# Performance work log

Hardware: AMD Instinct MI355X
Metric: run time of the kernel (lower is better)

The kernel has to match this reference:

```python
import jax, jax.numpy as jnp
import numpy as np
from jax import lax

EPS = 1e-05
Q = 4          # window size (hard-coded in BotBlock)
HEADS = 4
DIM = 16       # bottleneck(64) // heads(4)


def conv3x3(x, w, b):
    # x: [N,C,H,W], w: [O,I,3,3]
    y = lax.conv_general_dilated(x, w, (1, 1), ((1, 1), (1, 1)),
                                 dimension_numbers=('NCHW', 'OIHW', 'NCHW'))
    return y + b[None, :, None, None]


def batchnorm(x, gamma, beta):
    # training-mode BN: batch statistics over (N,H,W), biased variance
    m = jnp.mean(x, axis=(0, 2, 3), keepdims=True)
    v = jnp.var(x, axis=(0, 2, 3), keepdims=True)
    xn = (x - m) * lax.rsqrt(v + EPS)
    return xn * gamma[None, :, None, None] + beta[None, :, None, None]


def rel_to_abs(x):
    # x: [B, H, L, 2L-1] -> [B, H, L, L] via pad/reshape trick
    B, H, L, _ = x.shape
    x = jnp.pad(x, ((0, 0), (0, 0), (0, 0), (0, 1)))          # [B,H,L,2L]
    flat = x.reshape(B, H, -1)                                  # [B,H,2L*L]
    flat = jnp.pad(flat, ((0, 0), (0, 0), (0, L - 1)))
    final = flat.reshape(B, H, L + 1, 2 * L - 1)
    return final[:, :, :L, L - 1:]                              # [B,H,L,L]


def relative_logits_1d(q, rel_k, perm):
    # q: [b, n, h, w, d], rel_k: [2w-1, d]
    b, n, h, w, d = q.shape
    rl = jnp.einsum('bnhwd,md->bnhwm', q, rel_k)
    rl = rl.reshape(b, n * h, w, 2 * w - 1)
    rl = rel_to_abs(rl)                                         # [b, n*h, w, w]
    rl = rl.reshape(b, n, h, w, w)
    rl = jnp.broadcast_to(rl[:, :, :, None], (b, n, h, h, w, w))
    return jnp.transpose(rl, perm)


def rel_pos_attention(q, k, v, rel_w, rel_h):
    # q,k,v: [b, heads, h, w, d]
    b, n, h, w, d = q.shape
    q = q * (d ** -0.5)
    logits = jnp.einsum('bnhwd,bnpqd->bnhwpq', q, k)
    logits = logits + relative_logits_1d(q, rel_w, (0, 1, 2, 4, 3, 5))
    logits = logits + relative_logits_1d(jnp.transpose(q, (0, 1, 3, 2, 4)),
                                         rel_h, (0, 1, 4, 2, 5, 3))
    weights = jax.nn.softmax(logits.reshape(b, n, h, w, h * w), axis=-1)
    weights = weights.reshape(b, n, h, w, h, w)
    out = jnp.einsum('bnhwpq,bnpqd->bhwnd', weights, v)         # [b,h,w,n,d]
    return out.reshape(b, h, w, n * d)                          # fold heads


def setup_inputs() -> dict:
    key = jax.random.key(0)
    ks = jax.random.split(key, 16)
    C_in, C_bot, C_out = 64, 64, 256
    inp = {
        'x': jax.random.normal(ks[0], (2, C_in, 256, 256), jnp.float32),
        'conv1_w': jax.random.normal(ks[1], (C_bot, C_in, 3, 3), jnp.float32) * 0.05,
        'conv1_b': jnp.zeros((C_bot,), jnp.float32),
        'bn1_g': jnp.ones((C_bot,), jnp.float32),
        'bn1_b': jnp.zeros((C_bot,), jnp.float32),
        'wq': jax.random.normal(ks[2], (C_bot, HEADS, DIM), jnp.float32) * 0.01,
        'wk': jax.random.normal(ks[3], (C_bot, HEADS, DIM), jnp.float32) * 0.01,
        'wv': jax.random.normal(ks[4], (C_bot, HEADS, DIM), jnp.float32) * 0.01,
        'rel_w': jax.random.normal(ks[5], (2 * Q - 1, DIM), jnp.float32) * (DIM ** -0.5),
        'rel_h': jax.random.normal(ks[6], (2 * Q - 1, DIM), jnp.float32) * (DIM ** -0.5),
        'bn2_g': jnp.ones((C_bot,), jnp.float32),
        'bn2_b': jnp.zeros((C_bot,), jnp.float32),
        'conv3_w': jax.random.normal(ks[7], (C_out, C_bot, 3, 3), jnp.float32) * 0.05,
        'conv3_b': jnp.zeros((C_out,), jnp.float32),
        # NOTE: original init_zero=True zeros bn3 gamma; we randomize it so the
        # output (and gradients) are non-trivial for kernel correctness checks.
        'bn3_g': jax.random.normal(ks[8], (C_out,), jnp.float32),
        'bn3_b': jnp.zeros((C_out,), jnp.float32),
    }
    return inp


def reference(x, conv1_w, conv1_b, bn1_g, bn1_b, wq, wk, wv, rel_w, rel_h,
              bn2_g, bn2_b, conv3_w, conv3_b, bn3_g, bn3_b):
    N, C, H, W = x.shape
    P_h, P_w = H // Q, W // Q
    # raw memory reinterpretation into 4x4 blocks (matches torch .reshape)
    xb = x.reshape(N * P_h * P_w, C, Q, Q)
    out = jax.nn.relu(batchnorm(conv3x3(xb, conv1_w, conv1_b), bn1_g, bn1_b))
    # GroupPointWise projections: NCHW -> NHWC then einsum
    feat = jnp.transpose(out, (0, 2, 3, 1))                     # [b,h,w,c]
    q = jnp.einsum('bhwc,cnp->bnhwp', feat, wq)
    k = jnp.einsum('bhwc,cnp->bnhwp', feat, wk)
    v = jnp.einsum('bhwc,cnp->bnhwp', feat, wv)
    o = rel_pos_attention(q, k, v, rel_w, rel_h)                # [b,h,w,c]
    o = jnp.transpose(o, (0, 3, 1, 2))                          # NCHW
    o = jax.nn.relu(batchnorm(o, bn2_g, bn2_b))
    o = batchnorm(conv3x3(o, conv3_w, conv3_b), bn3_g, bn3_b)   # no act
    C1 = o.shape[1]
    o = o.reshape(N, C1, H, W)
    return jax.nn.relu(o)
```

## Files before the change

### kernel.cpp

```cpp
#include <hip/hip_runtime.h>
#include <stdint.h>


#define EPSV 1e-5f
#define INV_N (1.0f / 131072.0f)

typedef unsigned short u16;
typedef __attribute__((ext_vector_type(8))) short short8b;
typedef __attribute__((ext_vector_type(4))) float f32x4;

__device__ __forceinline__ u16 f2bf(float f) {
  unsigned u = __float_as_uint(f);
  u += 0x7fffu + ((u >> 16) & 1u);
  return (u16)(u >> 16);
}
__device__ __forceinline__ float bf2f(u16 h) {
  return __uint_as_float((unsigned)h << 16);
}

__device__ __forceinline__ float bn_scale(const float* __restrict__ acc,
                                          const float* __restrict__ gam,
                                          const float* __restrict__ bet,
                                          int C, int c, float& shift) {
  float S = acc[c], S2 = acc[C + c];
  float mean = S * INV_N;
  float var  = S2 * INV_N - mean * mean;
  float rstd = rsqrtf(var + EPSV);
  float sc = gam[c] * rstd;
  shift = bet[c] - mean * sc;
  return sc;
}

__global__ __launch_bounds__(256) void prep_kernel(const float* __restrict__ w1,
                                                   const float* __restrict__ w3,
                                                   const float* __restrict__ wq,
                                                   const float* __restrict__ wk,
                                                   const float* __restrict__ wv,
                                                   u16* __restrict__ wp1,
                                                   u16* __restrict__ wp3,
                                                   u16* __restrict__ wqkvT) {
  int i = blockIdx.x * 256 + threadIdx.x;
  const int tot1 = 18 * 64 * 40;
  const int tot3 = 9 * 256 * 64;
  if (i < tot1) {
    int ch = i / (64 * 40); int r = i - ch * 64 * 40; int o = r / 40; int kk = r - o * 40;
    float v = 0.f;
    if (kk < 32) { int k = ch * 32 + kk; int tap = k >> 6; int c = k & 63;
                   v = w1[o * 576 + c * 9 + tap]; }
    wp1[i] = f2bf(v);
  } else if (i < tot1 + tot3) {
    int j = i - tot1;
    int tap = j >> 14; int r = j & 16383; int o = r >> 6; int c = r & 63;
    wp3[j] = f2bf(w3[o * 576 + c * 9 + tap]);
  } else if (i < tot1 + tot3 + 192 * 64) {
    int j = i - tot1 - tot3;
    int oc = j >> 6, c = j & 63;
    const float* src = (oc < 64) ? wq : (oc < 128) ? wk : wv;
    wqkvT[j] = f2bf(src[(c << 6) + (oc & 63)]);
  }
}

__global__ __launch_bounds__(256) void conv1_kernel(const float* __restrict__ x,
                                                    const u16* __restrict__ wp,
                                                    u16* __restrict__ bufb,
                                                    float* __restrict__ partials1) {
  __shared__ __align__(16) char featA[257 * 128];
  __shared__ __align__(16) char ldsW[2][64 * 80];
  const int t = threadIdx.x;
  const int lane = t & 63, w = t >> 6;
  const int lrow = lane & 15, lk = lane >> 4;
  const int wm = w >> 1, wn = w & 1;
  const size_t Mbase = (size_t)blockIdx.x * 256;

  int rel[9];
  {
    const int pi = lrow >> 2, pj = lrow & 3;
#pragma unroll
    for (int tap = 0; tap < 9; ++tap) {
      const int ti = tap / 3, tj = tap - ti * 3;
      int si = pi + ti - 1, sj = pj + tj - 1;
      bool valid = ((unsigned)si < 4u) && ((unsigned)sj < 4u);
      rel[tap] = valid ? ((si * 4 + sj) << 7) : (1 << 24);
    }
  }

#pragma unroll
  for (int i = 0; i < 16; ++i) {
    float4 v = *reinterpret_cast<const float4*>(x + Mbase * 64 + i * 1024 + t * 4);
    const int c = t >> 2, p0 = (t & 3) * 4;
    float vv[4] = {v.x, v.y, v.z, v.w};
#pragma unroll
    for (int j = 0; j < 4; ++j) {
      int row = i * 16 + p0 + j;
      int byte = row * 128 + ((((c >> 3) ^ (row & 7)) << 4) | ((c & 7) << 1));
      *reinterpret_cast<u16*>(featA + byte) = f2bf(vv[j]);
    }
  }
  if (t < 8) *reinterpret_cast<uint4*>(featA + 256 * 128 + t * 16) = uint4{0, 0, 0, 0};

  uint4 s0, s1;
  {
    const u16* sp = wp;
    s0 = *reinterpret_cast<const uint4*>(sp + (size_t)t * 8);
    if (t < 64) s1 = *reinterpret_cast<const uint4*>(sp + (size_t)(t + 256) * 8);
    *reinterpret_cast<uint4*>(ldsW[0] + t * 16) = s0;
    if (t < 64) *reinterpret_cast<uint4*>(ldsW[0] + (t + 256) * 16) = s1;
  }
  __syncthreads();

  f32x4 acc[8][2] = {};
#pragma unroll
  for (int chn = 0; chn < 18; ++chn) {
    const int cur = chn & 1;
    const int tap = chn >> 1, kk = chn & 1;
    if (chn + 1 < 18) {
      const u16* sp = wp + (chn + 1) * 2560;
      s0 = *reinterpret_cast<const uint4*>(sp + (size_t)t * 8);
      if (t < 64) s1 = *reinterpret_cast<const uint4*>(sp + (size_t)(t + 256) * 8);
    }
    const int kkg = (kk << 6) | (lk << 4);
    short8b bw[2];
#pragma unroll
    for (int n = 0; n < 2; ++n)
      bw[n] = *reinterpret_cast<const short8b*>(ldsW[cur] + (wn * 32 + n * 16 + lrow) * 80 + lk * 16);
#pragma unroll
    for (int m = 0; m < 8; ++m) {
      int ad = ((wm * 128 + m * 16) << 7) + rel[tap];
      ad = ad < 32768 ? ad : 32768;
      ad += (kkg ^ ((ad >> 3) & 0x70));
      short8b af = *reinterpret_cast<const short8b*>(featA + ad);
#pragma unroll
      for (int n = 0; n < 2; ++n)
        acc[m][n] = __builtin_amdgcn_mfma_f32_16x16x32_bf16(af, bw[n], acc[m][n], 0, 0, 0);
    }
    if (chn + 1 < 18) {
      *reinterpret_cast<uint4*>(ldsW[cur ^ 1] + t * 16) = s0;
      if (t < 64) *reinterpret_cast<uint4*>(ldsW[cur ^ 1] + (t + 256) * 16) = s1;
    }
    __syncthreads();
  }

#pragma unroll
  for (int m = 0; m < 8; ++m) {
    const size_t rowg0 = Mbase + wm * 128 + m * 16 + lk * 4;
#pragma unroll
    for (int n = 0; n < 2; ++n) {
      const int o = wn * 32 + n * 16 + lrow;
#pragma unroll
      for (int r = 0; r < 4; ++r)
        bufb[(rowg0 + r) * 64 + o] = f2bf(acc[m][n][r]);
    }
  }

  float* pst = reinterpret_cast<float*>(featA);
  if (t < 128) pst[t] = 0.f;
  __syncthreads();
#pragma unroll
  for (int n = 0; n < 2; ++n) {
    float s = 0.f, s2 = 0.f;
#pragma unroll
    for (int m = 0; m < 8; ++m)
#pragma unroll
      for (int r = 0; r < 4; ++r) {
        float v = acc[m][n][r];
        s += v; s2 = fmaf(v, v, s2);
      }
    s += __shfl_xor(s, 16); s2 += __shfl_xor(s2, 16);
    s += __shfl_xor(s, 32); s2 += __shfl_xor(s2, 32);
    if (lk == 0) {
      const int o = wn * 32 + n * 16 + lrow;
      atomicAdd(&pst[o], s);
      atomicAdd(&pst[64 + o], s2);
    }
  }
  __syncthreads();
  if (t < 128) partials1[(size_t)blockIdx.x * 128 + t] = pst[t];
}

__global__ __launch_bounds__(256) void reduce12_kernel(const float* __restrict__ p,
                                                       float* __restrict__ acc, int nrows) {
  const int c = blockIdx.x, t = threadIdx.x;
  float s = 0.f;
  for (int i = t; i < nrows; i += 256) s += p[(size_t)i * 128 + c];
#pragma unroll
  for (int off = 32; off > 0; off >>= 1) s += __shfl_down(s, off);
  __shared__ float red[4];
  if ((t & 63) == 0) red[t >> 6] = s;
  __syncthreads();
  if (t == 0) acc[c] = red[0] + red[1] + red[2] + red[3];
}

#define QSTR 24
#define NSTR 400
#define KOFF 1600
#define VOFF 3200
#define USTR 4800

__global__ __launch_bounds__(256) void attn_kernel(u16* __restrict__ buf,
                                                   const u16* __restrict__ wqkvT,
                                                   const float* __restrict__ relw,
                                                   const float* __restrict__ relh,
                                                   const float* __restrict__ acc1,
                                                   const float* __restrict__ g1,
                                                   const float* __restrict__ b1,
                                                   float* __restrict__ partials2) {
  __shared__ float scsh[64][2];
  __shared__ float pstA[128];
  __shared__ __align__(16) u16 feat_l[4][16 * 64];
  __shared__ __align__(16) u16 qkv_l[4][USTR];
  const int t = threadIdx.x, u = t >> 6, lane = t & 63;
  const size_t b = (size_t)blockIdx.x * 4 + u;

  if (t < 64) {
    float sh; float sc = bn_scale(acc1, g1, b1, 64, t, sh);
    scsh[t][0] = sc; scsh[t][1] = sh;
  }
  if (t < 128) pstA[t] = 0.f;
  __syncthreads();

  {
    const int pos = lane >> 2, cq = lane & 3;
    const u16* src = buf + b * 1024 + pos * 64 + cq * 16;
    short8b v0 = *reinterpret_cast<const short8b*>(src);
    short8b v1 = *reinterpret_cast<const short8b*>(src + 8);
    short8b p0, p1;
#pragma unroll
    for (int j = 0; j < 8; ++j) {
      const int c0 = cq * 16 + j, c1 = cq * 16 + 8 + j;
      p0[j] = (short)f2bf(fmaxf(fmaf(bf2f((u16)v0[j]), scsh[c0][0], scsh[c0][1]), 0.f));
      p1[j] = (short)f2bf(fmaxf(fmaf(bf2f((u16)v1[j]), scsh[c1][0], scsh[c1][1]), 0.f));
    }
    const int g0 = (cq * 2) ^ (pos & 7), g1g = (cq * 2 + 1) ^ (pos & 7);
    *reinterpret_cast<short8b*>(&feat_l[u][pos * 64 + g0 * 8]) = p0;
    *reinterpret_cast<short8b*>(&feat_l[u][pos * 64 + g1g * 8]) = p1;
  }

  const int dq = lane & 15, lk = lane >> 4;
  short8b afr[2];
#pragma unroll
  for (int ch = 0; ch < 2; ++ch) {
    const int kg = ch * 4 + lk;
    afr[ch] = *reinterpret_cast<const short8b*>(&feat_l[u][dq * 64 + ((kg ^ (dq & 7)) * 8)]);
  }
#pragma unroll
  for (int ct = 0; ct < 12; ++ct) {
    f32x4 d = {0.f, 0.f, 0.f, 0.f};
#pragma unroll
    for (int ch = 0; ch < 2; ++ch) {
      short8b bfr = *reinterpret_cast<const short8b*>(&wqkvT[(ct * 16 + dq) * 64 + ch * 32 + lk * 8]);
      d = __builtin_amdgcn_mfma_f32_16x16x32_bf16(afr[ch], bfr, d, 0, 0, 0);
    }
    u16* dst;
    float scl = 1.f;
    if (ct < 4)      { dst = &qkv_l[u][ct * NSTR];              scl = 0.25f; }
    else if (ct < 8) { dst = &qkv_l[u][KOFF + (ct - 4) * NSTR]; }
    else             { dst = &qkv_l[u][VOFF + (ct - 8) * NSTR]; }
#pragma unroll
    for (int r = 0; r < 4; ++r)
      dst[(lk * 4 + r) * QSTR + dq] = f2bf(d[r] * scl);
  }

  const int n = lk, qp = dq;
  const int qi = qp >> 2, qj = qp & 3;
  float q_[16];
  {
    const u16* qrow = &qkv_l[u][n * NSTR + qp * QSTR];
    short8b qa = *reinterpret_cast<const short8b*>(&qrow[0]);
    short8b qb = *reinterpret_cast<const short8b*>(&qrow[8]);
#pragma unroll
    for (int j = 0; j < 8; ++j) { q_[j] = bf2f((u16)qa[j]); q_[8 + j] = bf2f((u16)qb[j]); }
  }
  float rwq[4], rhq[4];
  {
    const float* rwp = relw + (3 - qj) * 16;
    const float* rhp = relh + (3 - qi) * 16;
#pragma unroll
    for (int m = 0; m < 4; ++m) {
      float a1 = 0.f, a2 = 0.f;
#pragma unroll
      for (int d2 = 0; d2 < 16; ++d2) {
        a1 = fmaf(q_[d2], rwp[m * 16 + d2], a1);
        a2 = fmaf(q_[d2], rhp[m * 16 + d2], a2);
      }
      rwq[m] = a1; rhq[m] = a2;
    }
  }
  float lo[16]; float mx = -1e30f;
  const u16* kb = &qkv_l[u][KOFF + n * NSTR];
#pragma unroll
  for (int kp = 0; kp < 16; ++kp) {
    short8b k0 = *reinterpret_cast<const short8b*>(&kb[kp * QSTR]);
    short8b k1 = *reinterpret_cast<const short8b*>(&kb[kp * QSTR + 8]);
    float s = rwq[kp & 3] + rhq[kp >> 2];
#pragma unroll
    for (int j = 0; j < 8; ++j) {
      s = fmaf(q_[j], bf2f((u16)k0[j]), s);
      s = fmaf(q_[8 + j], bf2f((u16)k1[j]), s);
    }
    lo[kp] = s; mx = fmaxf(mx, s);
  }
  float ssum = 0.f;
#pragma unroll
  for (int kp = 0; kp < 16; ++kp) { float e = __expf(lo[kp] - mx); lo[kp] = e; ssum += e; }
  const float inv = 1.0f / ssum;
  float ov[16];
#pragma unroll
  for (int j = 0; j < 16; ++j) ov[j] = 0.f;
  const u16* vb = &qkv_l[u][VOFF + n * NSTR];
#pragma unroll
  for (int kp = 0; kp < 16; ++kp) {
    short8b v0 = *reinterpret_cast<const short8b*>(&vb[kp * QSTR]);
    short8b v1 = *reinterpret_cast<const short8b*>(&vb[kp * QSTR + 8]);
    const float wgt = lo[kp];
#pragma unroll
    for (int j = 0; j < 8; ++j) {
      ov[j] = fmaf(wgt, bf2f((u16)v0[j]), ov[j]);
      ov[8 + j] = fmaf(wgt, bf2f((u16)v1[j]), ov[8 + j]);
    }
  }
#pragma unroll
  for (int j = 0; j < 16; ++j) ov[j] *= inv;

  {
    short8b o0, o1;
#pragma unroll
    for (int j = 0; j < 8; ++j) {
      o0[j] = (short)f2bf(ov[j]);
      o1[j] = (short)f2bf(ov[8 + j]);
    }
    u16* dstb = buf + b * 1024 + qp * 64 + (n << 4);
    *reinterpret_cast<short8b*>(dstb) = o0;
    *reinterpret_cast<short8b*>(dstb + 8) = o1;
  }

  {
    float* fl = reinterpret_cast<float*>(&qkv_l[u][0]);
#pragma unroll
    for (int j = 0; j < 16; ++j) fl[qp * 69 + n * 16 + j] = ov[j];
    const int c = lane;
    float s = 0.f, s2 = 0.f;
#pragma unroll
    for (int pos = 0; pos < 16; ++pos) {
      float v = fl[pos * 69 + c];
      s += v; s2 = fmaf(v, v, s2);
    }
    atomicAdd(&pstA[c], s);
    atomicAdd(&pstA[64 + c], s2);
  }
  __syncthreads();
  if (t < 128) partials2[(size_t)blockIdx.x * 128 + t] = pstA[t];
}

__global__ __launch_bounds__(256, 2) void conv3_kernel(const u16* __restrict__ src,
                                                       const u16* __restrict__ wp,
                                                       const float* __restrict__ acc2,
                                                       const float* __restrict__ g2,
                                                       const float* __restrict__ b2,
                                                       float* __restrict__ out,
                                                       float* __restrict__ partials3) {
  __shared__ __align__(16) u16 featB[257 * 64];
  __shared__ __align__(16) u16 ldsW[2][128 * 64];
  __shared__ float scsh[128];
  const int t = threadIdx.x;
  const int lane = t & 63, w = t >> 6;
  const int lrow = lane & 15, lk = lane >> 4;
  const int wm = w >> 1, wn = w & 1;
  const int Nbase = blockIdx.x * 256;
  const int ohalf = blockIdx.y;

  int rel[9];
  {
    const int pi = lrow >> 2, pj = lrow & 3;
#pragma unroll
    for (int tap = 0; tap < 9; ++tap) {
      const int ti = tap / 3, tj = tap - ti * 3;
      int si = pi + ti - 1, sj = pj + tj - 1;
      bool valid = ((unsigned)si < 4u) && ((unsigned)sj < 4u);
      rel[tap] = valid ? ((si * 4 + sj) << 7) : (1 << 24);
    }
  }

  if (t < 64) {
    float sh; float sc = bn_scale(acc2, g2, b2, 64, t, sh);
    scsh[t * 2] = sc; scsh[t * 2 + 1] = sh;
  }

  const int so = t >> 1, shalf = t & 1, so7 = so & 7;
  {
    const u16* wsrc = wp + ohalf * 8192 + so * 64 + shalf * 32;
    uint4 w0 = *reinterpret_cast<const uint4*>(wsrc);
    uint4 w1 = *reinterpret_cast<const uint4*>(wsrc + 8);
    uint4 w2 = *reinterpret_cast<const uint4*>(wsrc + 16);
    uint4 w3v = *reinterpret_cast<const uint4*>(wsrc + 24);
    char* dst = (char*)ldsW[0] + so * 128;
    const int gb = shalf * 4;
    *reinterpret_cast<uint4*>(dst + (((gb + 0) ^ so7) << 4)) = w0;
    *reinterpret_cast<uint4*>(dst + (((gb + 1) ^ so7) << 4)) = w1;
    *reinterpret_cast<uint4*>(dst + (((gb + 2) ^ so7) << 4)) = w2;
    *reinterpret_cast<uint4*>(dst + (((gb + 3) ^ so7) << 4)) = w3v;
  }
  __syncthreads();

  {
    const u16* srow = src + (size_t)(Nbase + t) * 64;
    char* drow = (char*)featB + t * 128;
    const int r7 = t & 7;
#pragma unroll
    for (int g = 0; g < 8; ++g) {
      short8b v = *reinterpret_cast<const short8b*>(srow + g * 8);
      short8b pk;
#pragma unroll
      for (int j = 0; j < 8; ++j) {
        const int c = g * 8 + j;
        pk[j] = (short)f2bf(fmaxf(fmaf(bf2f((u16)v[j]), scsh[c * 2], scsh[c * 2 + 1]), 0.f));
      }
      *reinterpret_cast<short8b*>(drow + ((g ^ r7) << 4)) = pk;
    }
  }
  if (t < 8) *reinterpret_cast<uint4*>((char*)featB + 32768 + t * 16) = uint4{0, 0, 0, 0};

  uint4 r0, r1, r2, r3v;
  {
    const u16* wsrc = wp + 16384 + ohalf * 8192 + so * 64 + shalf * 32;
    r0 = *reinterpret_cast<const uint4*>(wsrc);
    r1 = *reinterpret_cast<const uint4*>(wsrc + 8);
    r2 = *reinterpret_cast<const uint4*>(wsrc + 16);
    r3v = *reinterpret_cast<const uint4*>(wsrc + 24);
  }
  __syncthreads();

  f32x4 acc[4][8] = {};
  const char* fB = (const char*)featB;
  const int swzA0 = (lk << 4) ^ ((lrow & 7) << 4);
  const int swzA1 = (64 | (lk << 4)) ^ ((lrow & 7) << 4);

#pragma unroll
  for (int tap = 0; tap < 9; ++tap) {
    const int cur = tap & 1;
    const char* lW = (const char*)ldsW[cur];
    short8b aw0[4], aw1[4];
#pragma unroll
    for (int m = 0; m < 4; ++m) {
      const int rowoff = (wm * 64 + m * 16 + lrow) << 7;
      aw0[m] = *reinterpret_cast<const short8b*>(lW + rowoff + swzA0);
      aw1[m] = *reinterpret_cast<const short8b*>(lW + rowoff + swzA1);
    }
#pragma unroll
    for (int n = 0; n < 8; ++n) {
      int ad0 = ((wn * 128 + n * 16) << 7) + rel[tap];
      ad0 = ad0 < 32768 ? ad0 : 32768;
      const int swz = (ad0 >> 3) & 0x70;
      short8b bf0 = *reinterpret_cast<const short8b*>(fB + ad0 + ((lk << 4) ^ swz));
      short8b bf1 = *reinterpret_cast<const short8b*>(fB + ad0 + ((64 | (lk << 4)) ^ swz));
#pragma unroll
      for (int m = 0; m < 4; ++m) {
        acc[m][n] = __builtin_amdgcn_mfma_f32_16x16x32_bf16(aw0[m], bf0, acc[m][n], 0, 0, 0);
        acc[m][n] = __builtin_amdgcn_mfma_f32_16x16x32_bf16(aw1[m], bf1, acc[m][n], 0, 0, 0);
      }
    }
    if (tap < 8) {
      char* dst = (char*)ldsW[cur ^ 1] + so * 128;
      const int gb = shalf * 4;
      *reinterpret_cast<uint4*>(dst + (((gb + 0) ^ so7) << 4)) = r0;
      *reinterpret_cast<uint4*>(dst + (((gb + 1) ^ so7) << 4)) = r1;
      *reinterpret_cast<uint4*>(dst + (((gb + 2) ^ so7) << 4)) = r2;
      *reinterpret_cast<uint4*>(dst + (((gb + 3) ^ so7) << 4)) = r3v;
      if (tap < 7) {
        const u16* wsrc = wp + (tap + 2) * 16384 + ohalf * 8192 + so * 64 + shalf * 32;
        r0 = *reinterpret_cast<const uint4*>(wsrc);
        r1 = *reinterpret_cast<const uint4*>(wsrc + 8);
        r2 = *reinterpret_cast<const uint4*>(wsrc + 16);
        r3v = *reinterpret_cast<const uint4*>(wsrc + 24);
      }
    }
    __syncthreads();
  }

#pragma unroll
  for (int m = 0; m < 4; ++m) {
    const int o = ohalf * 128 + wm * 64 + m * 16 + lk * 4;
#pragma unroll
    for (int n = 0; n < 8; ++n) {
      const int colg = Nbase + wn * 128 + n * 16 + lrow;
      const int b = colg >> 4, p = colg & 15;
      float* dst = out + (size_t)b * 4096 + (size_t)o * 16 + p;
#pragma unroll
      for (int r = 0; r < 4; ++r)
        dst[r * 16] = acc[m][n][r];
    }
  }

  float* pst = reinterpret_cast<float*>(featB);
  pst[t] = 0.f;
  __syncthreads();
#pragma unroll
  for (int m = 0; m < 4; ++m) {
#pragma unroll
    for (int r = 0; r < 4; ++r) {
      float s = 0.f, s2 = 0.f;
#pragma unroll
      for (int n = 0; n < 8; ++n) {
        float v = acc[m][n][r];
        s += v; s2 = fmaf(v, v, s2);
      }
      s += __shfl_xor(s, 1); s2 += __shfl_xor(s2, 1);
      s += __shfl_xor(s, 2); s2 += __shfl_xor(s2, 2);
      s += __shfl_xor(s, 4); s2 += __shfl_xor(s2, 4);
      s += __shfl_xor(s, 8); s2 += __shfl_xor(s2, 8);
      if (lrow == 0) {
        const int ch = wm * 64 + m * 16 + lk * 4 + r;
        atomicAdd(&pst[ch], s);
        atomicAdd(&pst[128 + ch], s2);
      }
    }
  }
  __syncthreads();
  partials3[((size_t)(ohalf * 512 + blockIdx.x)) * 256 + t] = pst[t];
}

__global__ __launch_bounds__(256) void reduce3_kernel(const float* __restrict__ p,
                                                      float* __restrict__ acc3) {
  const int c2 = blockIdx.x, t = threadIdx.x;
  const int kind = c2 >> 8, c = c2 & 255;
  const int h = c >> 7, chl = c & 127;
  float s = 0.f;
  for (int i = t; i < 512; i += 256)
    s += p[((size_t)(h * 512 + i)) * 256 + kind * 128 + chl];
#pragma unroll
  for (int off = 32; off > 0; off >>= 1) s += __shfl_down(s, off);
  __shared__ float red[4];
  if ((t & 63) == 0) red[t >> 6] = s;
  __syncthreads();
  if (t == 0) acc3[kind * 256 + c] = red[0] + red[1] + red[2] + red[3];
}

__global__ __launch_bounds__(256) void final_kernel(float* __restrict__ out,
                                                    const float* __restrict__ acc3,
                                                    const float* __restrict__ g3,
                                                    const float* __restrict__ b3) {
  const size_t i = ((size_t)blockIdx.x * 256 + threadIdx.x) * 4;
  const int c = (int)((i >> 4) & 255);
  float sh; const float sc = bn_scale(acc3, g3, b3, 256, c, sh);
  float4 v = *reinterpret_cast<float4*>(out + i);
  v.x = fmaxf(fmaf(v.x, sc, sh), 0.f);
  v.y = fmaxf(fmaf(v.y, sc, sh), 0.f);
  v.z = fmaxf(fmaf(v.z, sc, sh), 0.f);
  v.w = fmaxf(fmaf(v.w, sc, sh), 0.f);
  *reinterpret_cast<float4*>(out + i) = v;
}

extern "C" void kernel_launch(void* const* d_in, const int* in_sizes, int n_in,
                              void* d_out, int out_size, void* d_ws, size_t ws_size,
                              hipStream_t stream) {
  const float* x   = (const float*)d_in[0];
  const float* w1  = (const float*)d_in[1];
  const float* g1  = (const float*)d_in[3];
  const float* bb1 = (const float*)d_in[4];
  const float* wq  = (const float*)d_in[5];
  const float* wk  = (const float*)d_in[6];
  const float* wv  = (const float*)d_in[7];
  const float* rw  = (const float*)d_in[8];
  const float* rh  = (const float*)d_in[9];
  const float* g2  = (const float*)d_in[10];
  const float* bb2 = (const float*)d_in[11];
  const float* w3  = (const float*)d_in[12];
  const float* g3  = (const float*)d_in[14];
  const float* bb3 = (const float*)d_in[15];
  float* out = (float*)d_out;
  float* ws  = (float*)d_ws;

  u16*   bufb   = (u16*)ws;
  u16*   wp1    = bufb + 8388608;
  u16*   wp3    = wp1 + 46080;
  u16*   wqkvT  = wp3 + 147456;
  float* acc1   = ws + 4297216;
  float* acc2   = acc1 + 128;
  float* acc3   = acc2 + 128;
  float* part1  = acc3 + 512;
  float* part2  = part1 + 65536;
  float* part3  = part2 + 262144;

  prep_kernel<<<804, 256, 0, stream>>>(w1, w3, wq, wk, wv, wp1, wp3, wqkvT);
  conv1_kernel<<<512, 256, 0, stream>>>(x, wp1, bufb, part1);
  reduce12_kernel<<<128, 256, 0, stream>>>(part1, acc1, 512);
  attn_kernel<<<2048, 256, 0, stream>>>(bufb, wqkvT, rw, rh, acc1, g1, bb1, part2);
  reduce12_kernel<<<128, 256, 0, stream>>>(part2, acc2, 2048);
  conv3_kernel<<<dim3(512, 2), 256, 0, stream>>>(bufb, wp3, acc2, g2, bb2, out, part3);
  reduce3_kernel<<<512, 256, 0, stream>>>(part3, acc3);
  final_kernel<<<32768, 256, 0, stream>>>(out, acc3, g3, bb3);
}
```

Before: 172.6 us.

## Store conv3 pre-BN output as bf16 intermediate and keep attention QKV in fp32 LDS

The conv3 kernel now writes its pre-BN output as bf16 into a new workspace buffer instead of fp32 into the output. The final BN+ReLU kernel then reads that bf16 buffer and writes fp32 output, which halves the intermediate write and read traffic. Separately, the attention kernel keeps Q/K/V in fp32 shared memory with XOR-swizzled layouts, using float4 reads and no bf16 conversions. The trade-offs are lower precision on the conv3 intermediate, more LDS per block in attention (possibly lower occupancy), and a larger workspace.

```diff
diff --git a/kernel.cpp b/kernel.cpp
--- a/kernel.cpp
+++ b/kernel.cpp
@@ -190,12 +190,6 @@
   if (t == 0) acc[c] = red[0] + red[1] + red[2] + red[3];
 }
 
-#define QSTR 24
-#define NSTR 400
-#define KOFF 1600
-#define VOFF 3200
-#define USTR 4800
-
 __global__ __launch_bounds__(256) void attn_kernel(u16* __restrict__ buf,
                                                    const u16* __restrict__ wqkvT,
                                                    const float* __restrict__ relw,
@@ -206,10 +200,11 @@
                                                    float* __restrict__ partials2) {
   __shared__ float scsh[64][2];
   __shared__ float pstA[128];
-  __shared__ __align__(16) u16 feat_l[4][16 * 64];
-  __shared__ __align__(16) u16 qkv_l[4][USTR];
+  __shared__ __align__(16) u16 feat_l[4][1024];
+  __shared__ __align__(16) float qkvf[4][3264];
   const int t = threadIdx.x, u = t >> 6, lane = t & 63;
   const size_t b = (size_t)blockIdx.x * 4 + u;
+  float* Wf = qkvf[u];
 
   if (t < 64) {
     float sh; float sc = bn_scale(acc1, g1, b1, 64, t, sh);
@@ -250,25 +245,25 @@
       short8b bfr = *reinterpret_cast<const short8b*>(&wqkvT[(ct * 16 + dq) * 64 + ch * 32 + lk * 8]);
       d = __builtin_amdgcn_mfma_f32_16x16x32_bf16(afr[ch], bfr, d, 0, 0, 0);
     }
-    u16* dst;
-    float scl = 1.f;
-    if (ct < 4)      { dst = &qkv_l[u][ct * NSTR];              scl = 0.25f; }
-    else if (ct < 8) { dst = &qkv_l[u][KOFF + (ct - 4) * NSTR]; }
-    else             { dst = &qkv_l[u][VOFF + (ct - 8) * NSTR]; }
-#pragma unroll
-    for (int r = 0; r < 4; ++r)
-      dst[(lk * 4 + r) * QSTR + dq] = f2bf(d[r] * scl);
+    if (ct < 4) {
+      float* dst = Wf + ct * 280;
+#pragma unroll
+      for (int r = 0; r < 4; ++r) dst[(lk * 4 + r) * 17 + dq] = d[r] * 0.25f;
+    } else {
+      float* dst = (ct < 8) ? (Wf + 1120 + (ct - 4) * 264) : (Wf + 2176 + (ct - 8) * 264);
+      const int cp = dq ^ (lk << 2);
+#pragma unroll
+      for (int r = 0; r < 4; ++r) dst[(lk * 4 + r) * 16 + cp] = d[r];
+    }
   }
 
   const int n = lk, qp = dq;
   const int qi = qp >> 2, qj = qp & 3;
   float q_[16];
   {
-    const u16* qrow = &qkv_l[u][n * NSTR + qp * QSTR];
-    short8b qa = *reinterpret_cast<const short8b*>(&qrow[0]);
-    short8b qb = *reinterpret_cast<const short8b*>(&qrow[8]);
-#pragma unroll
-    for (int j = 0; j < 8; ++j) { q_[j] = bf2f((u16)qa[j]); q_[8 + j] = bf2f((u16)qb[j]); }
+    const float* qb = Wf + n * 280 + qp * 17;
+#pragma unroll
+    for (int d2 = 0; d2 < 16; ++d2) q_[d2] = qb[d2];
   }
   float rwq[4], rhq[4];
   {
@@ -286,16 +281,17 @@
     }
   }
   float lo[16]; float mx = -1e30f;
-  const u16* kb = &qkv_l[u][KOFF + n * NSTR];
+  const float* kbase = Wf + 1120 + n * 264;
 #pragma unroll
   for (int kp = 0; kp < 16; ++kp) {
-    short8b k0 = *reinterpret_cast<const short8b*>(&kb[kp * QSTR]);
-    short8b k1 = *reinterpret_cast<const short8b*>(&kb[kp * QSTR + 8]);
+    const float4* kr = reinterpret_cast<const float4*>(kbase + kp * 16);
     float s = rwq[kp & 3] + rhq[kp >> 2];
 #pragma unroll
-    for (int j = 0; j < 8; ++j) {
-      s = fmaf(q_[j], bf2f((u16)k0[j]), s);
-      s = fmaf(q_[8 + j], bf2f((u16)k1[j]), s);
+    for (int g = 0; g < 4; ++g) {
+      float4 kv = kr[g];
+      const int lg = (g ^ (kp >> 2)) * 4;
+      s = fmaf(q_[lg], kv.x, s); s = fmaf(q_[lg + 1], kv.y, s);
+      s = fmaf(q_[lg + 2], kv.z, s); s = fmaf(q_[lg + 3], kv.w, s);
     }
     lo[kp] = s; mx = fmaxf(mx, s);
   }
@@ -306,16 +302,19 @@
   float ov[16];
 #pragma unroll
   for (int j = 0; j < 16; ++j) ov[j] = 0.f;
-  const u16* vb = &qkv_l[u][VOFF + n * NSTR];
+  const float* vbase = Wf + 2176 + n * 264;
 #pragma unroll
   for (int kp = 0; kp < 16; ++kp) {
-    short8b v0 = *reinterpret_cast<const short8b*>(&vb[kp * QSTR]);
-    short8b v1 = *reinterpret_cast<const short8b*>(&vb[kp * QSTR + 8]);
+    const float4* vr = reinterpret_cast<const float4*>(vbase + kp * 16);
     const float wgt = lo[kp];
 #pragma unroll
-    for (int j = 0; j < 8; ++j) {
-      ov[j] = fmaf(wgt, bf2f((u16)v0[j]), ov[j]);
-      ov[8 + j] = fmaf(wgt, bf2f((u16)v1[j]), ov[8 + j]);
+    for (int g = 0; g < 4; ++g) {
+      float4 vv = vr[g];
+      const int lg = (g ^ (kp >> 2)) * 4;
+      ov[lg] = fmaf(wgt, vv.x, ov[lg]);
+      ov[lg + 1] = fmaf(wgt, vv.y, ov[lg + 1]);
+      ov[lg + 2] = fmaf(wgt, vv.z, ov[lg + 2]);
+      ov[lg + 3] = fmaf(wgt, vv.w, ov[lg + 3]);
     }
   }
 #pragma unroll
@@ -334,7 +333,7 @@
   }
 
   {
-    float* fl = reinterpret_cast<float*>(&qkv_l[u][0]);
+    float* fl = Wf;
 #pragma unroll
     for (int j = 0; j < 16; ++j) fl[qp * 69 + n * 16 + j] = ov[j];
     const int c = lane;
@@ -356,7 +355,7 @@
                                                        const float* __restrict__ acc2,
                                                        const float* __restrict__ g2,
                                                        const float* __restrict__ b2,
-                                                       float* __restrict__ out,
+                                                       u16* __restrict__ y3b,
                                                        float* __restrict__ partials3) {
   __shared__ __align__(16) u16 featB[257 * 64];
   __shared__ __align__(16) u16 ldsW[2][128 * 64];
@@ -483,10 +482,10 @@
     for (int n = 0; n < 8; ++n) {
       const int colg = Nbase + wn * 128 + n * 16 + lrow;
       const int b = colg >> 4, p = colg & 15;
-      float* dst = out + (size_t)b * 4096 + (size_t)o * 16 + p;
+      u16* dst = y3b + (size_t)b * 4096 + (size_t)o * 16 + p;
 #pragma unroll
       for (int r = 0; r < 4; ++r)
-        dst[r * 16] = acc[m][n][r];
+        dst[r * 16] = f2bf(acc[m][n][r]);
     }
   }
 
@@ -534,19 +533,26 @@
   if (t == 0) acc3[kind * 256 + c] = red[0] + red[1] + red[2] + red[3];
 }
 
-__global__ __launch_bounds__(256) void final_kernel(float* __restrict__ out,
+__global__ __launch_bounds__(256) void final_kernel(const u16* __restrict__ y3b,
+                                                    float* __restrict__ out,
                                                     const float* __restrict__ acc3,
                                                     const float* __restrict__ g3,
                                                     const float* __restrict__ b3) {
-  const size_t i = ((size_t)blockIdx.x * 256 + threadIdx.x) * 4;
+  const size_t i = ((size_t)blockIdx.x * 256 + threadIdx.x) * 8;
   const int c = (int)((i >> 4) & 255);
   float sh; const float sc = bn_scale(acc3, g3, b3, 256, c, sh);
-  float4 v = *reinterpret_cast<float4*>(out + i);
-  v.x = fmaxf(fmaf(v.x, sc, sh), 0.f);
-  v.y = fmaxf(fmaf(v.y, sc, sh), 0.f);
-  v.z = fmaxf(fmaf(v.z, sc, sh), 0.f);
-  v.w = fmaxf(fmaf(v.w, sc, sh), 0.f);
-  *reinterpret_cast<float4*>(out + i) = v;
+  short8b v = *reinterpret_cast<const short8b*>(y3b + i);
+  float4 o0, o1;
+  o0.x = fmaxf(fmaf(bf2f((u16)v[0]), sc, sh), 0.f);
+  o0.y = fmaxf(fmaf(bf2f((u16)v[1]), sc, sh), 0.f);
+  o0.z = fmaxf(fmaf(bf2f((u16)v[2]), sc, sh), 0.f);
+  o0.w = fmaxf(fmaf(bf2f((u16)v[3]), sc, sh), 0.f);
+  o1.x = fmaxf(fmaf(bf2f((u16)v[4]), sc, sh), 0.f);
+  o1.y = fmaxf(fmaf(bf2f((u16)v[5]), sc, sh), 0.f);
+  o1.z = fmaxf(fmaf(bf2f((u16)v[6]), sc, sh), 0.f);
+  o1.w = fmaxf(fmaf(bf2f((u16)v[7]), sc, sh), 0.f);
+  *reinterpret_cast<float4*>(out + i) = o0;
+  *reinterpret_cast<float4*>(out + i + 4) = o1;
 }
 
 extern "C" void kernel_launch(void* const* d_in, const int* in_sizes, int n_in,
@@ -570,10 +576,11 @@
   float* ws  = (float*)d_ws;
 
   u16*   bufb   = (u16*)ws;
-  u16*   wp1    = bufb + 8388608;
+  u16*   y3b    = bufb + 8388608;
+  u16*   wp1    = y3b + 33554432;
   u16*   wp3    = wp1 + 46080;
   u16*   wqkvT  = wp3 + 147456;
-  float* acc1   = ws + 4297216;
+  float* acc1   = ws + 21074432;
   float* acc2   = acc1 + 128;
   float* acc3   = acc2 + 128;
   float* part1  = acc3 + 512;
@@ -585,7 +592,7 @@
   reduce12_kernel<<<128, 256, 0, stream>>>(part1, acc1, 512);
   attn_kernel<<<2048, 256, 0, stream>>>(bufb, wqkvT, rw, rh, acc1, g1, bb1, part2);
   reduce12_kernel<<<128, 256, 0, stream>>>(part2, acc2, 2048);
-  conv3_kernel<<<dim3(512, 2), 256, 0, stream>>>(bufb, wp3, acc2, g2, bb2, out, part3);
+  conv3_kernel<<<dim3(512, 2), 256, 0, stream>>>(bufb, wp3, acc2, g2, bb2, y3b, part3);
   reduce3_kernel<<<512, 256, 0, stream>>>(part3, acc3);
-  final_kernel<<<32768, 256, 0, stream>>>(out, acc3, g3, bb3);
-}
+  final_kernel<<<16384, 256, 0, stream>>>(y3b, out, acc3, g3, bb3);
+}
```

New measurement: 163.9 us. 5.1% less time.
